# Performance work log

Hardware: AMD Instinct MI355X
Metric: run time of the kernel (lower is better)

The kernel has to match this reference:

```python
import jax, jax.numpy as jnp
import numpy as np

BETA = 0.25      # commitment loss weight
DECAY = 0.99     # EMA decay
EPS = 1e-5       # Laplace smoothing for counts


def setup_inputs() -> dict:
    key = jax.random.key(0)
    k1, k2, k3 = jax.random.split(key, 3)
    B, d, h, w, K = 16, 64, 64, 64, 1024
    z_e = jax.random.normal(k1, (B, d, h, w), dtype=jnp.float32)
    codebook = jax.random.normal(k2, (K, d), dtype=jnp.float32)
    ema_count = jnp.ones((K,), dtype=jnp.float32)
    ema_sum = jax.random.normal(k3, (K, d), dtype=jnp.float32)
    return {"z_e": z_e, "codebook": codebook, "ema_count": ema_count, "ema_sum": ema_sum}


def reference(z_e, codebook, ema_count, ema_sum):
    B, d, h, w = z_e.shape
    K = codebook.shape[0]
    # [B,d,h,w] -> [N,d], N = B*h*w
    z_flat = jnp.transpose(z_e, (0, 2, 3, 1)).reshape(-1, d)
    # squared euclidean distances [N,K]
    dist = (jnp.sum(z_flat * z_flat, axis=1, keepdims=True)
            - 2.0 * (z_flat @ codebook.T)
            + jnp.sum(codebook * codebook, axis=1)[None, :])
    indices = jnp.argmin(dist, axis=1)                      # [N] int
    e_k = codebook[indices].reshape(B, h, w, d).transpose(0, 3, 1, 2)  # [B,d,h,w]

    # --- EMA codebook update (training mode, no grad) ---
    zf = jax.lax.stop_gradient(z_flat)
    counts = jax.ops.segment_sum(jnp.ones((zf.shape[0],), dtype=zf.dtype), indices, num_segments=K)
    sums = jax.ops.segment_sum(zf, indices, num_segments=K)
    new_count = ema_count * DECAY + (1.0 - DECAY) * counts
    new_sum = ema_sum * DECAY + (1.0 - DECAY) * sums
    n = jnp.sum(new_count)
    count_s = (new_count + EPS) / (n + K * EPS) * n
    new_codebook = new_sum / count_s[:, None]

    # straight-through estimator
    e_k_ste = z_e + jax.lax.stop_gradient(e_k - z_e)
    L_commit = (jnp.mean((z_e - jax.lax.stop_gradient(e_k)) ** 2)
                + BETA * jnp.mean((jax.lax.stop_gradient(z_e) - e_k) ** 2))
    return (e_k_ste, indices.reshape(B, h, w), L_commit, new_codebook, new_count, new_sum)
```

## Files before the change

### kernel.cpp

```cpp
#include <hip/hip_runtime.h>
#include <hip/hip_bf16.h>
#include <hip/hip_fp16.h>

#define NB 16
#define DD 64
#define HW 4096
#define NTOT 65536
#define KC 1024

#define O_EK   0
#define O_IDX  4194304
#define O_L    4259840
#define O_CB   4259841
#define O_CNT  4325377
#define O_SUM  4326401

#define WS_IDX    0
#define WS_LCPART 65536
#define WS_N      66048
#define WS_CNORM  66560
#define WS_PSUM   67584
#define WS_PCNT   329728
#define WS_FLGC   333824
#define WS_FLGL   334336
#define WS_CBH    399360
#define WS_CBL    432128

#define MARGIN 0.002f
#define MAXFLG 32

typedef _Float16 v8h __attribute__((ext_vector_type(8)));
typedef float    v4f __attribute__((ext_vector_type(4)));

__global__ __launch_bounds__(256) void k_pre(const float* __restrict__ cb,
                                             const float* __restrict__ ema_count,
                                             float* __restrict__ cnorm,
                                             float* __restrict__ n_ws,
                                             unsigned short* __restrict__ cbh,
                                             unsigned short* __restrict__ cbl) {
    const int t = threadIdx.x;
    const int w = (blockIdx.x * 256 + t) >> 6;
    const int l = t & 63;
    float s = 0.f;
    if (l < 16) {
        float4 v = *(const float4*)(cb + (size_t)w * DD + l * 4);
        s = v.x * v.x + v.y * v.y + v.z * v.z + v.w * v.w;
    }
#pragma unroll
    for (int m = 1; m <= 8; m <<= 1) s += __shfl_xor(s, m, 64);
    if (l == 0) cnorm[w] = s;

    const int e4 = blockIdx.x * 256 + t;
    if (e4 < 16384) {
        float4 v4 = ((const float4*)cb)[e4];
        __half hx = __float2half(v4.x), hy = __float2half(v4.y),
               hz = __float2half(v4.z), hw2 = __float2half(v4.w);
        ushort4 h4 = { __half_as_ushort(hx), __half_as_ushort(hy),
                       __half_as_ushort(hz), __half_as_ushort(hw2) };
        ((ushort4*)cbh)[e4] = h4;
        ushort4 l4 = { __half_as_ushort(__float2half(v4.x - __half2float(hx))),
                       __half_as_ushort(__float2half(v4.y - __half2float(hy))),
                       __half_as_ushort(__float2half(v4.z - __half2float(hz))),
                       __half_as_ushort(__float2half(v4.w - __half2float(hw2))) };
        ((ushort4*)cbl)[e4] = l4;
    }

    if (blockIdx.x == 0) {
        __shared__ float red[256];
        red[t] = ema_count[t] + ema_count[t + 256] + ema_count[t + 512] + ema_count[t + 768];
        __syncthreads();
        for (int s2 = 128; s2 >= 1; s2 >>= 1) {
            if (t < s2) red[t] += red[t + s2];
            __syncthreads();
        }
        if (t == 0) n_ws[0] = 0.99f * red[0] + 0.01f * 65536.0f;
    }
}

__global__ __launch_bounds__(256) void k_argmin(const float* __restrict__ z_e,
                                                const unsigned short* __restrict__ cbh,
                                                const unsigned short* __restrict__ cbl,
                                                const float* __restrict__ cnorm,
                                                int* __restrict__ idx_ws,
                                                int* __restrict__ flg_cnt,
                                                int* __restrict__ flg_list,
                                                float* __restrict__ out) {
    __shared__ __align__(16) unsigned short A2h[8][128][8];
    __shared__ __align__(16) unsigned short A2l[8][128][8];
    __shared__ __align__(16) unsigned short B2h[8][64][8];
    __shared__ __align__(16) unsigned short B2l[8][64][8];
    __shared__ int idx_lds[128];
    __shared__ int flagrows[128];
    __shared__ int nflag;

    float* slab = (float*)&B2h[0][0][0];

    const int t  = threadIdx.x;
    const int n0 = blockIdx.x * 128;
    const int b   = n0 >> 12;
    const int hw0 = n0 & 4095;
    const float* zbase = z_e + (size_t)b * (DD * HW) + hw0;

    if (t == 0) nflag = 0;

    for (int sl = 0; sl < 4; ++sl) {
        __syncthreads();
#pragma unroll
        for (int s = 0; s < 2; ++s) {
            int idx = t + s * 256;
            int j   = idx >> 5;
            int m4  = (idx & 31) << 2;
            float4 v = *(const float4*)(zbase + (size_t)(sl * 16 + j) * HW + m4);
            *(float4*)&slab[j * 128 + m4] = v;
        }
        __syncthreads();
        {
            const int chl = t >> 7;
            const int m   = t & 127;
            const int ch  = sl * 2 + chl;
            unsigned hv[4], lv[4];
#pragma unroll
            for (int p = 0; p < 4; ++p) {
                float v0 = slab[(chl * 8 + 2 * p    ) * 128 + m];
                float v1 = slab[(chl * 8 + 2 * p + 1) * 128 + m];
                __half h0 = __float2half(v0), h1 = __float2half(v1);
                __half l0 = __float2half(v0 - __half2float(h0));
                __half l1 = __float2half(v1 - __half2float(h1));
                hv[p] = (unsigned)__half_as_ushort(h0) | ((unsigned)__half_as_ushort(h1) << 16);
                lv[p] = (unsigned)__half_as_ushort(l0) | ((unsigned)__half_as_ushort(l1) << 16);
            }
            uint4 hq = {hv[0], hv[1], hv[2], hv[3]};
            uint4 lq = {lv[0], lv[1], lv[2], lv[3]};
            *(uint4*)&A2h[ch][m][0] = hq;
            *(uint4*)&A2l[ch][m][0] = lq;
        }
    }
    __syncthreads();

    const int w    = t >> 6;
    const int lane = t & 63;
    const int c    = lane & 15;
    const int q    = lane >> 4;

    v8h Afh[2][2], Afl[2][2];
#pragma unroll
    for (int g = 0; g < 2; ++g) {
        int m = 32 * w + 16 * g + c;
#pragma unroll
        for (int s = 0; s < 2; ++s) {
            Afh[g][s] = *(const v8h*)&A2h[s * 4 + q][m][0];
            Afl[g][s] = *(const v8h*)&A2l[s * 4 + q][m][0];
        }
    }

    float m1v[2][4], m2v[2][4]; int m1i[2][4];
#pragma unroll
    for (int g = 0; g < 2; ++g)
#pragma unroll
        for (int r = 0; r < 4; ++r) { m1v[g][r] = 3.4e38f; m2v[g][r] = 3.4e38f; m1i[g][r] = 0; }

    for (int kt = 0; kt < 16; ++kt) {
        __syncthreads();
#pragma unroll
        for (int s2 = 0; s2 < 2; ++s2) {
            int idx  = t + s2 * 256;
            int ch   = idx >> 6;
            int code = idx & 63;
            size_t gsrc = ((size_t)(kt * 64 + code)) * 64 + ch * 8;
            *(uint4*)&B2h[ch][code][0] = *(const uint4*)(cbh + gsrc);
            *(uint4*)&B2l[ch][code][0] = *(const uint4*)(cbl + gsrc);
        }
        __syncthreads();

#pragma unroll
        for (int sub = 0; sub < 4; ++sub) {
            const int cl = sub * 16 + c;
            v8h Bfh0 = *(const v8h*)&B2h[q][cl][0];
            v8h Bfh1 = *(const v8h*)&B2h[4 + q][cl][0];
            v8h Bfl0 = *(const v8h*)&B2l[q][cl][0];
            v8h Bfl1 = *(const v8h*)&B2l[4 + q][cl][0];
            const int kg = kt * 64 + cl;
            float cnc = cnorm[kg];
#pragma unroll
            for (int g = 0; g < 2; ++g) {
                v4f acc = {0.f, 0.f, 0.f, 0.f};
                acc = __builtin_amdgcn_mfma_f32_16x16x32_f16(Afh[g][0], Bfh0, acc, 0, 0, 0);
                acc = __builtin_amdgcn_mfma_f32_16x16x32_f16(Afh[g][1], Bfh1, acc, 0, 0, 0);
                acc = __builtin_amdgcn_mfma_f32_16x16x32_f16(Afh[g][0], Bfl0, acc, 0, 0, 0);
                acc = __builtin_amdgcn_mfma_f32_16x16x32_f16(Afh[g][1], Bfl1, acc, 0, 0, 0);
                acc = __builtin_amdgcn_mfma_f32_16x16x32_f16(Afl[g][0], Bfh0, acc, 0, 0, 0);
                acc = __builtin_amdgcn_mfma_f32_16x16x32_f16(Afl[g][1], Bfh1, acc, 0, 0, 0);
#pragma unroll
                for (int r = 0; r < 4; ++r) {
                    float v = fmaf(-2.0f, acc[r], cnc);
                    bool better = v < m1v[g][r];
                    m2v[g][r] = better ? m1v[g][r] : fminf(m2v[g][r], v);
                    m1i[g][r] = better ? kg : m1i[g][r];
                    m1v[g][r] = better ? v : m1v[g][r];
                }
            }
        }
    }

#pragma unroll
    for (int g = 0; g < 2; ++g)
#pragma unroll
        for (int r = 0; r < 4; ++r) {
            float a = m1v[g][r], b2 = m2v[g][r]; int ii = m1i[g][r];
#pragma unroll
            for (int mask = 1; mask <= 8; mask <<= 1) {
                float ov = __shfl_xor(a, mask, 64);
                int   oi = __shfl_xor(ii, mask, 64);
                float o2 = __shfl_xor(b2, mask, 64);
                bool take = (ov < a) || (ov == a && oi < ii);
                float loser = take ? a : ov;
                b2 = fminf(fminf(b2, o2), loser);
                a  = take ? ov : a;
                ii = take ? oi : ii;
            }
            if (c == 0) {
                int row = 32 * w + 16 * g + q * 4 + r;
                idx_lds[row] = ii;
                if ((b2 - a) < MARGIN) { int p = atomicAdd(&nflag, 1); flagrows[p] = row; }
            }
        }
    __syncthreads();

    int nf = nflag; if (nf > MAXFLG) nf = MAXFLG;
    if (t == 0) flg_cnt[blockIdx.x] = nf;
    if (t < nf) flg_list[blockIdx.x * MAXFLG + t] = flagrows[t];

    if (t < 128) {
        int bi = idx_lds[t];
        out[O_IDX + n0 + t] = (float)bi;
        idx_ws[n0 + t] = bi;
    }
}

__global__ __launch_bounds__(256) void k_fix(const float* __restrict__ z_e,
                                             const float* __restrict__ cb,
                                             const float* __restrict__ cnorm,
                                             const int* __restrict__ flg_cnt,
                                             const int* __restrict__ flg_list,
                                             int* __restrict__ idx_ws,
                                             float* __restrict__ out) {
    const int blk = blockIdx.x;
    const int nf = flg_cnt[blk];
    if (nf == 0) return;
    __shared__ float redv4[4];
    __shared__ int   redi4[4];
    const int t = threadIdx.x;
    const int lane = t & 63, w = t >> 6;
    const int n0 = blk * 128;
    const int b   = n0 >> 12;
    const int hw0 = n0 & 4095;

    for (int f = 0; f < nf; ++f) {
        int row = flg_list[blk * MAXFLG + f];
        const float* zrow = z_e + (size_t)b * (DD * HW) + hw0 + row;
        float znr = 0.f;
        for (int j = 0; j < 64; ++j) { float v = zrow[(size_t)j * HW]; znr = fmaf(v, v, znr); }
        float best = 3.4e38f; int bi = 0;
#pragma unroll
        for (int c2 = 0; c2 < 4; ++c2) {
            int k = t * 4 + c2;
            const float* ck = cb + (size_t)k * DD;
            float acc = 0.f;
            for (int j = 0; j < 64; ++j) acc = fmaf(zrow[(size_t)j * HW], ck[j], acc);
            float v = (znr - 2.0f * acc) + cnorm[k];
            if (v < best) { best = v; bi = k; }
        }
#pragma unroll
        for (int mask = 1; mask <= 32; mask <<= 1) {
            float ov = __shfl_xor(best, mask, 64);
            int   oi = __shfl_xor(bi, mask, 64);
            if (ov < best || (ov == best && oi < bi)) { best = ov; bi = oi; }
        }
        if (lane == 0) { redv4[w] = best; redi4[w] = bi; }
        __syncthreads();
        if (t == 0) {
            float bv = redv4[0]; int bix = redi4[0];
#pragma unroll
            for (int w2 = 1; w2 < 4; ++w2)
                if (redv4[w2] < bv || (redv4[w2] == bv && redi4[w2] < bix)) { bv = redv4[w2]; bix = redi4[w2]; }
            idx_ws[n0 + row] = bix;
            out[O_IDX + n0 + row] = (float)bix;
        }
        __syncthreads();
    }
}

__global__ __launch_bounds__(1024) void k_out(const int* __restrict__ idx_ws,
                                              const float* __restrict__ z_e,
                                              const float* __restrict__ cb,
                                              float* __restrict__ psum,
                                              int* __restrict__ pcnt,
                                              float* __restrict__ lc_part,
                                              float* __restrict__ out) {
    __shared__ float acc[KC];
    __shared__ int bins[KC];
    __shared__ float cbj[KC];
    __shared__ float lcr[16];
    const int j = blockIdx.x & 63;
    const int c = blockIdx.x >> 6;
    const int t = threadIdx.x;
    acc[t] = 0.f;
    bins[t] = 0;
    cbj[t] = cb[(size_t)t * DD + j];
    __syncthreads();
    const float* zj = z_e + (size_t)j * HW;
    float* oj = out + O_EK + (size_t)j * HW;
    const int base = c * 16384;
    float lc = 0.f;
#pragma unroll
    for (int i = 0; i < 4; ++i) {
        int n4 = base + i * 4096 + t * 4;
        int b = n4 >> 12, hw = n4 & 4095;
        size_t zoff = (size_t)b * (DD * HW) + hw;
        float4 z4 = *(const float4*)(zj + zoff);
        int4   k4 = *(const int4*)(idx_ws + n4);
        float e0 = cbj[k4.x], e1 = cbj[k4.y], e2 = cbj[k4.z], e3 = cbj[k4.w];
        float4 o4 = { z4.x + (e0 - z4.x), z4.y + (e1 - z4.y),
                      z4.z + (e2 - z4.z), z4.w + (e3 - z4.w) };
        *(float4*)(oj + zoff) = o4;
        float d0 = z4.x - e0, d1 = z4.y - e1, d2 = z4.z - e2, d3 = z4.w - e3;
        lc = fmaf(d0, d0, lc); lc = fmaf(d1, d1, lc);
        lc = fmaf(d2, d2, lc); lc = fmaf(d3, d3, lc);
        atomicAdd(&acc[k4.x], z4.x);
        atomicAdd(&acc[k4.y], z4.y);
        atomicAdd(&acc[k4.z], z4.z);
        atomicAdd(&acc[k4.w], z4.w);
        if (j == 0) {
            atomicAdd(&bins[k4.x], 1); atomicAdd(&bins[k4.y], 1);
            atomicAdd(&bins[k4.z], 1); atomicAdd(&bins[k4.w], 1);
        }
    }
    __syncthreads();
    psum[(size_t)c * 65536 + j * 1024 + t] = acc[t];
    if (j == 0) pcnt[c * 1024 + t] = bins[t];
#pragma unroll
    for (int m = 32; m >= 1; m >>= 1) lc += __shfl_xor(lc, m, 64);
    if ((t & 63) == 0) lcr[t >> 6] = lc;
    __syncthreads();
    if (t == 0) {
        float s = 0.f;
#pragma unroll
        for (int u = 0; u < 16; ++u) s += lcr[u];
        lc_part[blockIdx.x] = s;
    }
}

__global__ __launch_bounds__(1024) void k_epi(const float* __restrict__ psum,
                                              const int* __restrict__ pcnt,
                                              const float* __restrict__ ema_sum,
                                              const float* __restrict__ ema_count,
                                              const float* __restrict__ n_ws,
                                              const float* __restrict__ lc_part,
                                              float* __restrict__ out) {
    const int t = threadIdx.x;
    const int e = blockIdx.x * 1024 + t;
    const int k = e >> 6, j = e & 63;
    float s4 = psum[j * 1024 + k] + psum[65536 + j * 1024 + k]
             + psum[131072 + j * 1024 + k] + psum[196608 + j * 1024 + k];
    float ns = ema_sum[e] * 0.99f + 0.01f * s4;
    out[O_SUM + e] = ns;
    int cnt = pcnt[k] + pcnt[1024 + k] + pcnt[2048 + k] + pcnt[3072 + k];
    float nc = ema_count[k] * 0.99f + 0.01f * (float)cnt;
    float n  = n_ws[0];
    float cs = (nc + 1e-5f) / (n + 1024.0f * 1e-5f) * n;
    out[O_CB + e] = ns / cs;
    if (blockIdx.x == 0) {
        int c2 = pcnt[t] + pcnt[1024 + t] + pcnt[2048 + t] + pcnt[3072 + t];
        out[O_CNT + t] = ema_count[t] * 0.99f + 0.01f * (float)c2;
    }
    if (blockIdx.x == 1) {
        __shared__ float red[512];
        if (t < 512) red[t] = (t < 256) ? lc_part[t] : 0.f;
        __syncthreads();
        for (int s = 256; s >= 1; s >>= 1) {
            if (t < s) red[t] += red[t + s];
            __syncthreads();
        }
        if (t == 0) out[O_L] = 1.25f * red[0] * (1.0f / 4194304.0f);
    }
}

extern "C" void kernel_launch(void* const* d_in, const int* in_sizes, int n_in,
                              void* d_out, int out_size, void* d_ws, size_t ws_size,
                              hipStream_t stream) {
    const float* z_e       = (const float*)d_in[0];
    const float* cb        = (const float*)d_in[1];
    const float* ema_count = (const float*)d_in[2];
    const float* ema_sum   = (const float*)d_in[3];
    float* out             = (float*)d_out;

    float* ws_f      = (float*)d_ws;
    int*   idx_ws    = (int*)d_ws;
    float* lc_part   = ws_f + WS_LCPART;
    float* n_ws      = ws_f + WS_N;
    float* cnorm_ws  = ws_f + WS_CNORM;
    float* psum      = ws_f + WS_PSUM;
    int*   pcnt      = (int*)(ws_f + WS_PCNT);
    int*   flg_cnt   = (int*)(ws_f + WS_FLGC);
    int*   flg_list  = (int*)(ws_f + WS_FLGL);
    unsigned short* cbh = (unsigned short*)(ws_f + WS_CBH);
    unsigned short* cbl = (unsigned short*)(ws_f + WS_CBL);

    k_pre<<<256, 256, 0, stream>>>(cb, ema_count, cnorm_ws, n_ws, cbh, cbl);
    k_argmin<<<NTOT / 128, 256, 0, stream>>>(z_e, cbh, cbl, cnorm_ws, idx_ws, flg_cnt, flg_list, out);
    k_fix<<<NTOT / 128, 256, 0, stream>>>(z_e, cb, cnorm_ws, flg_cnt, flg_list, idx_ws, out);
    k_out<<<256, 1024, 0, stream>>>(idx_ws, z_e, cb, psum, pcnt, lc_part, out);
    k_epi<<<64, 1024, 0, stream>>>(psum, pcnt, ema_sum, ema_count, n_ws, lc_part, out);
}
```

Before: 163.9 us.

## Double-buffer codebook tiles in LDS and prefetch next tile into registers

Codebook tiles in the argmin kernel now use two LDS buffers. The next tile's global loads are issued into registers before the MFMA work on the current tile, then written to the other buffer afterwards, so each iteration needs one barrier instead of two. The z_e staging also moves larger slabs in fewer passes (2 instead of 4). This trades extra LDS and registers, which may lower occupancy, for hiding global load latency behind compute.

```diff
diff --git a/kernel.cpp b/kernel.cpp
--- a/kernel.cpp
+++ b/kernel.cpp
@@ -87,13 +87,13 @@
                                                 float* __restrict__ out) {
     __shared__ __align__(16) unsigned short A2h[8][128][8];
     __shared__ __align__(16) unsigned short A2l[8][128][8];
-    __shared__ __align__(16) unsigned short B2h[8][64][8];
-    __shared__ __align__(16) unsigned short B2l[8][64][8];
+    __shared__ __align__(16) unsigned short B2h[2][8][64][8];
+    __shared__ __align__(16) unsigned short B2l[2][8][64][8];
     __shared__ int idx_lds[128];
     __shared__ int flagrows[128];
     __shared__ int nflag;
 
-    float* slab = (float*)&B2h[0][0][0];
+    float* slab = (float*)&B2h[0][0][0][0];
 
     const int t  = threadIdx.x;
     const int n0 = blockIdx.x * 128;
@@ -103,21 +103,23 @@
 
     if (t == 0) nflag = 0;
 
-    for (int sl = 0; sl < 4; ++sl) {
-        __syncthreads();
-#pragma unroll
-        for (int s = 0; s < 2; ++s) {
+    for (int sl = 0; sl < 2; ++sl) {
+        if (sl) __syncthreads();
+#pragma unroll
+        for (int s = 0; s < 4; ++s) {
             int idx = t + s * 256;
             int j   = idx >> 5;
             int m4  = (idx & 31) << 2;
-            float4 v = *(const float4*)(zbase + (size_t)(sl * 16 + j) * HW + m4);
+            float4 v = *(const float4*)(zbase + (size_t)(sl * 32 + j) * HW + m4);
             *(float4*)&slab[j * 128 + m4] = v;
         }
         __syncthreads();
-        {
-            const int chl = t >> 7;
-            const int m   = t & 127;
-            const int ch  = sl * 2 + chl;
+#pragma unroll
+        for (int s = 0; s < 2; ++s) {
+            int ss  = t + s * 256;
+            int chl = ss >> 7;
+            int m   = ss & 127;
+            int ch  = sl * 4 + chl;
             unsigned hv[4], lv[4];
 #pragma unroll
             for (int p = 0; p < 4; ++p) {
@@ -142,6 +144,11 @@
     const int c    = lane & 15;
     const int q    = lane >> 4;
 
+    const int ch0   = t >> 6;
+    const int code0 = t & 63;
+    const int ch1   = 4 + (t >> 6);
+    const int code1 = t & 63;
+
     v8h Afh[2][2], Afl[2][2];
 #pragma unroll
     for (int g = 0; g < 2; ++g) {
@@ -153,6 +160,16 @@
         }
     }
 
+    {
+        size_t g0 = ((size_t)code0) * 64 + ch0 * 8;
+        size_t g1 = ((size_t)code1) * 64 + ch1 * 8;
+        *(uint4*)&B2h[0][ch0][code0][0] = *(const uint4*)(cbh + g0);
+        *(uint4*)&B2l[0][ch0][code0][0] = *(const uint4*)(cbl + g0);
+        *(uint4*)&B2h[0][ch1][code1][0] = *(const uint4*)(cbh + g1);
+        *(uint4*)&B2l[0][ch1][code1][0] = *(const uint4*)(cbl + g1);
+    }
+    __syncthreads();
+
     float m1v[2][4], m2v[2][4]; int m1i[2][4];
 #pragma unroll
     for (int g = 0; g < 2; ++g)
@@ -160,25 +177,24 @@
         for (int r = 0; r < 4; ++r) { m1v[g][r] = 3.4e38f; m2v[g][r] = 3.4e38f; m1i[g][r] = 0; }
 
     for (int kt = 0; kt < 16; ++kt) {
-        __syncthreads();
-#pragma unroll
-        for (int s2 = 0; s2 < 2; ++s2) {
-            int idx  = t + s2 * 256;
-            int ch   = idx >> 6;
-            int code = idx & 63;
-            size_t gsrc = ((size_t)(kt * 64 + code)) * 64 + ch * 8;
-            *(uint4*)&B2h[ch][code][0] = *(const uint4*)(cbh + gsrc);
-            *(uint4*)&B2l[ch][code][0] = *(const uint4*)(cbl + gsrc);
-        }
-        __syncthreads();
+        const int cur = kt & 1, nxt = cur ^ 1;
+        uint4 ph0, pl0, ph1, pl1;
+        if (kt < 15) {
+            size_t g0 = ((size_t)((kt + 1) * 64 + code0)) * 64 + ch0 * 8;
+            size_t g1 = ((size_t)((kt + 1) * 64 + code1)) * 64 + ch1 * 8;
+            ph0 = *(const uint4*)(cbh + g0);
+            pl0 = *(const uint4*)(cbl + g0);
+            ph1 = *(const uint4*)(cbh + g1);
+            pl1 = *(const uint4*)(cbl + g1);
+        }
 
 #pragma unroll
         for (int sub = 0; sub < 4; ++sub) {
             const int cl = sub * 16 + c;
-            v8h Bfh0 = *(const v8h*)&B2h[q][cl][0];
-            v8h Bfh1 = *(const v8h*)&B2h[4 + q][cl][0];
-            v8h Bfl0 = *(const v8h*)&B2l[q][cl][0];
-            v8h Bfl1 = *(const v8h*)&B2l[4 + q][cl][0];
+            v8h Bfh0 = *(const v8h*)&B2h[cur][q][cl][0];
+            v8h Bfh1 = *(const v8h*)&B2h[cur][4 + q][cl][0];
+            v8h Bfl0 = *(const v8h*)&B2l[cur][q][cl][0];
+            v8h Bfl1 = *(const v8h*)&B2l[cur][4 + q][cl][0];
             const int kg = kt * 64 + cl;
             float cnc = cnorm[kg];
 #pragma unroll
@@ -200,6 +216,14 @@
                 }
             }
         }
+
+        if (kt < 15) {
+            *(uint4*)&B2h[nxt][ch0][code0][0] = ph0;
+            *(uint4*)&B2l[nxt][ch0][code0][0] = pl0;
+            *(uint4*)&B2h[nxt][ch1][code1][0] = ph1;
+            *(uint4*)&B2l[nxt][ch1][code1][0] = pl1;
+        }
+        __syncthreads();
     }
 
 #pragma unroll
```

Result: faster. 159.2 us, median of 2 (-2.9%).
